# Kernel optimization log

Hardware: AMD Instinct MI355X
Metric: run time of the kernel (lower is better)

The kernel has to match this reference:

```python
import jax, jax.numpy as jnp
import numpy as np

N_VOX = 200_000
C = 64
B, G = 2, 128  # batch size, grid resolution per axis
K = 27         # 3x3x3 kernel volume
EPS = 1e-5


def _build_coords_and_kernel_map(seed=0):
    """Build unique voxel coords on a [B,G,G,G] grid and the 27-offset kernel map.

    nbr[i, k] = row index of the voxel at coord[i] + offset[k], or N_VOX if absent
    (sentinel row that gathers zeros). This mirrors MinkowskiEngine's
    coordinate-hash in/out kernel maps for a stride-1 conv.
    """
    rng = np.random.default_rng(seed)
    total = B * G * G * G
    keys = np.sort(rng.choice(total, size=N_VOX, replace=False).astype(np.int64))
    z = keys % G
    y = (keys // G) % G
    x = (keys // (G * G)) % G
    b = keys // (G * G * G)
    offs = [(dx, dy, dz) for dx in (-1, 0, 1) for dy in (-1, 0, 1) for dz in (-1, 0, 1)]
    nbr = np.full((N_VOX, K), N_VOX, dtype=np.int64)
    for k, (dx, dy, dz) in enumerate(offs):
        nx, ny, nz = x + dx, y + dy, z + dz
        valid = (nx >= 0) & (nx < G) & (ny >= 0) & (ny < G) & (nz >= 0) & (nz < G)
        nkey = ((b * G + nx) * G + ny) * G + nz
        pos = np.clip(np.searchsorted(keys, nkey), 0, N_VOX - 1)
        found = valid & (keys[pos] == nkey)
        nbr[:, k] = np.where(found, pos, N_VOX)
    return jnp.asarray(nbr)


def setup_inputs() -> dict:
    key = jax.random.key(0)
    ks = jax.random.split(key, 12)
    w_scale = 1.0 / np.sqrt(K * C)
    inp = {
        "feats": jax.random.normal(ks[0], (N_VOX, C), jnp.float32),
        "nbr": _build_coords_and_kernel_map(),
        "W1": jax.random.normal(ks[1], (K, C, C), jnp.float32) * w_scale,
        "g1": 1.0 + 0.1 * jax.random.normal(ks[2], (C,), jnp.float32),
        "b1": 0.1 * jax.random.normal(ks[3], (C,), jnp.float32),
        "m1": 0.1 * jax.random.normal(ks[4], (C,), jnp.float32),
        "v1": jax.random.uniform(ks[5], (C,), jnp.float32, 0.5, 1.5),
        "W2": jax.random.normal(ks[6], (K, C, C), jnp.float32) * w_scale,
        "g2": 1.0 + 0.1 * jax.random.normal(ks[7], (C,), jnp.float32),
        "b2": 0.1 * jax.random.normal(ks[8], (C,), jnp.float32),
        "m2": 0.1 * jax.random.normal(ks[9], (C,), jnp.float32),
        "v2": jax.random.uniform(ks[10], (C,), jnp.float32, 0.5, 1.5),
    }
    return inp


def _bn(x, g, b, m, v):
    # MinkowskiBatchNorm, eval mode: per-channel affine with running stats
    return (x - m) * (g * jax.lax.rsqrt(v + EPS)) + b


def _sparse_conv(feats, nbr, W):
    # gather-GEMM-scatter sparse 3D conv over the precomputed kernel map.
    # Sentinel index N_VOX gathers the appended zero row (missing neighbor).
    fpad = jnp.concatenate([feats, jnp.zeros((1, feats.shape[1]), feats.dtype)], axis=0)
    out = jnp.zeros((feats.shape[0], W.shape[2]), feats.dtype)
    for k in range(W.shape[0]):  # fixed 27-tap loop (structural, not data dim)
        out = out + fpad[nbr[:, k]] @ W[k]
    return out


def reference(feats, nbr, W1, g1, b1, m1, v1, W2, g2, b2, m2, v2):
    h = jax.nn.relu(_bn(_sparse_conv(feats, nbr, W1), g1, b1, m1, v1))
    h = _bn(_sparse_conv(h, nbr, W2), g2, b2, m2, v2)
    # in_channels == out_channels and stride == 1 -> identity shortcut
    return jax.nn.relu(h + feats)
```

## Files before the change

kernel.cpp:

```cpp
#include <hip/hip_runtime.h>
#include <hip/hip_bf16.h>

#define NVOX 200000
#define NTAP 27
#define NSTR 68
#define OSTR 68

typedef __bf16          bf16x8 __attribute__((ext_vector_type(8)));
typedef unsigned short  u16x8  __attribute__((ext_vector_type(8)));
typedef float           f32x4  __attribute__((ext_vector_type(4)));

#define ROWB        128
#define FB_BYTES    ((size_t)(NVOX + 1) * ROWB)
#define WSHUF_BYTES (NTAP * 2 * 4 * 64 * 16)
#define FB_OFF      0
#define H_OFF       (FB_BYTES)
#define WS1_OFF     (2 * FB_BYTES)
#define WS2_OFF     (WS1_OFF + WSHUF_BYTES)
#define FLAG_OFF    (WS2_OFF + WSHUF_BYTES)

static __device__ __forceinline__ unsigned short f2bf_bits(float f) {
    __hip_bfloat16 h = __float2bfloat16(f);
    union { __hip_bfloat16 h; unsigned short u; } u; u.h = h; return u.u;
}
static __device__ __forceinline__ float bf2f(unsigned short s) {
    union { float f; unsigned u; } u; u.u = ((unsigned)s) << 16; return u.f;
}
static __device__ __forceinline__ float ld_param(const void* p, int c, int isbf) {
    return isbf ? bf2f(((const unsigned short*)p)[c]) : ((const float*)p)[c];
}
static __device__ __forceinline__ int wave_isbf(const unsigned* v1w) {
    int l = threadIdx.x & 63;
    int ok = 1;
    if (l < 32) {
        unsigned w = v1w[l], lo = w & 0xFFFFu, hi = w >> 16;
        ok = (lo >= 0x3F00u && lo <= 0x3FC0u && hi >= 0x3F00u && hi <= 0x3FC0u);
    }
    return __all(ok);
}

__global__ __launch_bounds__(256)
void prep_kernel(const void* __restrict__ feats,
                 const void* __restrict__ W1, const void* __restrict__ W2,
                 const unsigned* __restrict__ v1w, const unsigned* __restrict__ nbrw,
                 uint4* __restrict__ fbuf, uint4* __restrict__ hbuf,
                 uint4* __restrict__ Ws1, uint4* __restrict__ Ws2,
                 int* __restrict__ flags) {
    const int bx = blockIdx.x;
    if (bx < 6250) {
        const int isbf = wave_isbf(v1w);
        size_t t = (size_t)bx * 256 + threadIdx.x;
        if (isbf) {
            fbuf[t] = ((const uint4*)feats)[t];
        } else {
            float4 a = ((const float4*)feats)[2 * t];
            float4 b = ((const float4*)feats)[2 * t + 1];
            union { uint4 q; unsigned short u[8]; } o;
            o.u[0] = f2bf_bits(a.x); o.u[1] = f2bf_bits(a.y);
            o.u[2] = f2bf_bits(a.z); o.u[3] = f2bf_bits(a.w);
            o.u[4] = f2bf_bits(b.x); o.u[5] = f2bf_bits(b.y);
            o.u[6] = f2bf_bits(b.z); o.u[7] = f2bf_bits(b.w);
            fbuf[t] = o.q;
        }
    } else if (bx < 6358) {
        const int isbf = wave_isbf(v1w);
        int t = (bx - 6250) * 256 + threadIdx.x;
        const void* W = (t < 13824) ? W1 : W2;
        uint4* Ws     = (t < 13824) ? Ws1 : Ws2;
        int f = (t < 13824) ? t : t - 13824;
        int k  = f / 512;
        int r  = f % 512;
        int kc = r / 256;
        int r2 = r % 256;
        int nc = r2 / 64;
        int l  = r2 % 64;
        int quad = l >> 4, li = l & 15;
        unsigned short tmp[8];
#pragma unroll
        for (int j = 0; j < 8; ++j) {
            int off = k * 4096 + (kc * 32 + quad * 8 + j) * 64 + (nc * 16 + li);
            tmp[j] = isbf ? ((const unsigned short*)W)[off]
                          : f2bf_bits(((const float*)W)[off]);
        }
        uint4 v;
        v.x = (unsigned)tmp[0] | ((unsigned)tmp[1] << 16);
        v.y = (unsigned)tmp[2] | ((unsigned)tmp[3] << 16);
        v.z = (unsigned)tmp[4] | ((unsigned)tmp[5] << 16);
        v.w = (unsigned)tmp[6] | ((unsigned)tmp[7] << 16);
        Ws[f] = v;
    } else {
        int t = threadIdx.x;
        if (t < 64) {
            int isbf = wave_isbf(v1w);
            int n64ok = 1;
#pragma unroll
            for (int i = 0; i < 8; ++i)
                if (nbrw[2 * (t * 8 + i) + 1] != 0u) n64ok = 0;
            int n64 = __all(n64ok);
            if (t == 0) { flags[0] = isbf; flags[1] = n64; }
        }
        uint4 z = make_uint4(0u, 0u, 0u, 0u);
        if (t >= 64 && t < 72) fbuf[(size_t)NVOX * 8 + (t - 64)] = z;
        if (t >= 72 && t < 80) hbuf[(size_t)NVOX * 8 + (t - 72)] = z;
    }
}

#define STAGE(kk, bp) do {                                                  \
    int idx_ = nbrLDS[(kk) * NSTR + srow];                                  \
    const uint4* rp_ = srcV + (size_t)idx_ * 8;                             \
    uint4 v0_ = rp_[sf0];                                                   \
    uint4 v1_ = rp_[sf0 + 4];                                               \
    (bp)[ws0] = v0_;                                                        \
    (bp)[ws1] = v1_;                                                        \
} while (0)

#define LOADB(kk, B0, B1) do {                                              \
    B0 = Ws[(kk) * 512 + w * 64 + l];                                       \
    B1 = Ws[(kk) * 512 + 256 + w * 64 + l];                                 \
} while (0)

#define COMPUTE(kk, bp, B0, B1) do {                                        \
    _Pragma("unroll")                                                       \
    for (int g = 0; g < 4; ++g) {                                           \
        if ((mg[g] >> (kk)) & 1) {                                          \
            bf16x8 a0_ = *(const bf16x8*)((bp) + ro0[g]);                   \
            bf16x8 a1_ = *(const bf16x8*)((bp) + ro1[g]);                   \
            acc[g] = __builtin_amdgcn_mfma_f32_16x16x32_bf16(a0_, B0, acc[g], 0, 0, 0); \
            acc[g] = __builtin_amdgcn_mfma_f32_16x16x32_bf16(a1_, B1, acc[g], 0, 0, 0); \
        }                                                                   \
    }                                                                       \
} while (0)

__global__ __launch_bounds__(256, 6)
void conv_bn_kernel(const uint4* __restrict__ srcV,
                    const void* __restrict__ nbr,
                    const bf16x8* __restrict__ Ws,
                    const void* __restrict__ gg, const void* __restrict__ bb,
                    const void* __restrict__ mm, const void* __restrict__ vv,
                    const u16x8* __restrict__ resid,
                    const int* __restrict__ flags,
                    void* __restrict__ dst, int final_out) {
    __shared__ uint4 sm[1484];
    __shared__ int maskLDS[4];
    int*   nbrLDS = (int*)sm;
    uint4* at0    = sm + 459;
    uint4* at1    = at0 + 512;
    float* outLDS = (float*)sm;

    const int tid  = threadIdx.x;
    const int base = blockIdx.x * 64;
    const int isbf = flags[0];
    const int n64  = flags[1];

    if (tid < 4) maskLDS[tid] = 0;
    {
        for (int i = tid; i < NTAP * 64; i += 256) {
            int mvox = i / NTAP;
            int ktap = i - mvox * NTAP;
            long gi = (long)base * NTAP + i;
            int idx = n64 ? (int)((const long long*)nbr)[gi] : ((const int*)nbr)[gi];
            nbrLDS[ktap * NSTR + mvox] = idx;
        }
    }
    __syncthreads();

    if (tid < NTAP * 4) {
        int k = tid >> 2, g = tid & 3;
        const int4* p = (const int4*)&nbrLDS[k * NSTR + g * 16];
        int4 a = p[0], b = p[1], c = p[2], d = p[3];
        int mn = min(min(min(a.x, a.y), min(a.z, a.w)),
                     min(min(min(b.x, b.y), min(b.z, b.w)),
                         min(min(min(c.x, c.y), min(c.z, c.w)),
                             min(min(d.x, d.y), min(d.z, d.w)))));
        if (mn < NVOX) atomicOr(&maskLDS[g], 1 << k);
    }
    __syncthreads();

    const int w = tid >> 6, l = tid & 63;
    const int quad = l >> 4, li = l & 15;

    int mg[4];
#pragma unroll
    for (int g = 0; g < 4; ++g) mg[g] = __builtin_amdgcn_readfirstlane(maskLDS[g]);

    const int srow = tid & 63;
    const int sf0  = tid >> 6;
    const int ws0  = srow * 8 + ((sf0 + srow) & 7);
    const int ws1  = srow * 8 + ((sf0 + 4 + srow) & 7);
    int ro0[4], ro1[4];
#pragma unroll
    for (int g = 0; g < 4; ++g) {
        int row = g * 16 + li;
        ro0[g] = row * 8 + ((quad + row) & 7);
        ro1[g] = row * 8 + ((quad + 4 + row) & 7);
    }

    f32x4 acc[4];
#pragma unroll
    for (int g = 0; g < 4; ++g) acc[g] = (f32x4){0.f, 0.f, 0.f, 0.f};

    bf16x8 xB0, xB1, yB0, yB1;
    STAGE(0, at0);
    LOADB(0, xB0, xB1);
    __syncthreads();

    for (int k = 0; k < 26; k += 2) {
        STAGE(k + 1, at1);
        LOADB(k + 1, yB0, yB1);
        COMPUTE(k, at0, xB0, xB1);
        __syncthreads();
        STAGE(k + 2, at0);
        LOADB(k + 2, xB0, xB1);
        COMPUTE(k + 1, at1, yB0, yB1);
        __syncthreads();
    }
    COMPUTE(26, at0, xB0, xB1);

    const int c = w * 16 + li;
    float scale = ld_param(gg, c, isbf) * rsqrtf(ld_param(vv, c, isbf) + 1e-5f);
    float offs  = ld_param(bb, c, isbf) - ld_param(mm, c, isbf) * scale;

    __syncthreads();
#pragma unroll
    for (int g = 0; g < 4; ++g)
#pragma unroll
        for (int r = 0; r < 4; ++r)
            outLDS[(g * 16 + quad * 4 + r) * OSTR + c] = acc[g][r] * scale + offs;
    __syncthreads();

    {
        int trow = tid >> 2, cc = tid & 3;
        long grow = base + trow;
        const float4* lp = (const float4*)&outLDS[trow * OSTR + cc * 16];
        float4 q0 = lp[0], q1 = lp[1], q2 = lp[2], q3 = lp[3];
        float vals[16] = {q0.x, q0.y, q0.z, q0.w, q1.x, q1.y, q1.z, q1.w,
                          q2.x, q2.y, q2.z, q2.w, q3.x, q3.y, q3.z, q3.w};

        if (resid) {
            const u16x8* rp = resid + grow * 8 + cc * 2;
            u16x8 r0 = rp[0], r1 = rp[1];
#pragma unroll
            for (int j = 0; j < 8; ++j) { vals[j] += bf2f(r0[j]); vals[8 + j] += bf2f(r1[j]); }
        }
#pragma unroll
        for (int j = 0; j < 16; ++j) vals[j] = fmaxf(vals[j], 0.f);

        const int store_bf = (!final_out) || isbf;
        if (store_bf) {
            u16x8 o0, o1;
#pragma unroll
            for (int j = 0; j < 8; ++j) { o0[j] = f2bf_bits(vals[j]); o1[j] = f2bf_bits(vals[8 + j]); }
            u16x8* dp = (u16x8*)dst + grow * 8 + cc * 2;
            dp[0] = o0; dp[1] = o1;
        } else {
            float4* dp = (float4*)dst + grow * 16 + cc * 4;
            dp[0] = (float4){vals[0], vals[1], vals[2], vals[3]};
            dp[1] = (float4){vals[4], vals[5], vals[6], vals[7]};
            dp[2] = (float4){vals[8], vals[9], vals[10], vals[11]};
            dp[3] = (float4){vals[12], vals[13], vals[14], vals[15]};
        }
    }
}

extern "C" void kernel_launch(void* const* d_in, const int* in_sizes, int n_in,
                              void* d_out, int out_size, void* d_ws, size_t ws_size,
                              hipStream_t stream) {
    const void* feats = d_in[0];
    const void* nbr   = d_in[1];
    const void* W1    = d_in[2];
    const void* g1    = d_in[3];
    const void* b1    = d_in[4];
    const void* m1    = d_in[5];
    const void* v1    = d_in[6];
    const void* W2    = d_in[7];
    const void* g2    = d_in[8];
    const void* b2    = d_in[9];
    const void* m2    = d_in[10];
    const void* v2    = d_in[11];

    char* ws = (char*)d_ws;
    uint4* fbuf = (uint4*)(ws + FB_OFF);
    uint4* hbuf = (uint4*)(ws + H_OFF);
    uint4* Ws1  = (uint4*)(ws + WS1_OFF);
    uint4* Ws2  = (uint4*)(ws + WS2_OFF);
    int*   flags = (int*)(ws + FLAG_OFF);

    prep_kernel<<<dim3(6359), dim3(256), 0, stream>>>(
        feats, W1, W2, (const unsigned*)v1, (const unsigned*)nbr,
        fbuf, hbuf, Ws1, Ws2, flags);

    conv_bn_kernel<<<dim3(NVOX / 64), dim3(256), 0, stream>>>(
        fbuf, nbr, (const bf16x8*)Ws1, g1, b1, m1, v1,
        nullptr, flags, hbuf, 0);

    conv_bn_kernel<<<dim3(NVOX / 64), dim3(256), 0, stream>>>(
        hbuf, nbr, (const bf16x8*)Ws2, g2, b2, m2, v2,
        (const u16x8*)fbuf, flags, d_out, 1);
}
```

Baseline: 270.0 us.

## Fuse fp32-to-bf16 feature conversion into conv gather and prefetch neighbor rows into registers

Drops the separate pass that converted the whole fp32 feature tensor to a bf16 buffer. The first conv now gathers fp32 neighbor rows directly and converts them before writing to LDS, and the residual add reads fp32 feats directly. Missing neighbors point at a shared zero row, so the padded buffers are no longer needed. The gather is reorganized into global loads into registers issued one tap ahead, with the LDS write after the MFMA compute, to overlap gather latency with compute. This raises register pressure (launch bounds occupancy hint lowered from 6 to 5), and the first conv now gathers twice as many bytes per neighbor row.

```diff
diff --git a/kernel.cpp b/kernel.cpp
--- a/kernel.cpp
+++ b/kernel.cpp
@@ -11,13 +11,13 @@
 typedef float           f32x4  __attribute__((ext_vector_type(4)));
 
 #define ROWB        128
-#define FB_BYTES    ((size_t)(NVOX + 1) * ROWB)
+#define H_BYTES     ((size_t)NVOX * ROWB)
 #define WSHUF_BYTES (NTAP * 2 * 4 * 64 * 16)
-#define FB_OFF      0
-#define H_OFF       (FB_BYTES)
-#define WS1_OFF     (2 * FB_BYTES)
+#define H_OFF       0
+#define WS1_OFF     (H_BYTES)
 #define WS2_OFF     (WS1_OFF + WSHUF_BYTES)
-#define FLAG_OFF    (WS2_OFF + WSHUF_BYTES)
+#define ZROW_OFF    (WS2_OFF + WSHUF_BYTES)
+#define FLAG_OFF    (ZROW_OFF + 512)
 
 static __device__ __forceinline__ unsigned short f2bf_bits(float f) {
     __hip_bfloat16 h = __float2bfloat16(f);
@@ -40,58 +40,14 @@
 }
 
 __global__ __launch_bounds__(256)
-void prep_kernel(const void* __restrict__ feats,
-                 const void* __restrict__ W1, const void* __restrict__ W2,
+void prep_kernel(const void* __restrict__ W1, const void* __restrict__ W2,
                  const unsigned* __restrict__ v1w, const unsigned* __restrict__ nbrw,
-                 uint4* __restrict__ fbuf, uint4* __restrict__ hbuf,
                  uint4* __restrict__ Ws1, uint4* __restrict__ Ws2,
-                 int* __restrict__ flags) {
-    const int bx = blockIdx.x;
-    if (bx < 6250) {
-        const int isbf = wave_isbf(v1w);
-        size_t t = (size_t)bx * 256 + threadIdx.x;
-        if (isbf) {
-            fbuf[t] = ((const uint4*)feats)[t];
-        } else {
-            float4 a = ((const float4*)feats)[2 * t];
-            float4 b = ((const float4*)feats)[2 * t + 1];
-            union { uint4 q; unsigned short u[8]; } o;
-            o.u[0] = f2bf_bits(a.x); o.u[1] = f2bf_bits(a.y);
-            o.u[2] = f2bf_bits(a.z); o.u[3] = f2bf_bits(a.w);
-            o.u[4] = f2bf_bits(b.x); o.u[5] = f2bf_bits(b.y);
-            o.u[6] = f2bf_bits(b.z); o.u[7] = f2bf_bits(b.w);
-            fbuf[t] = o.q;
-        }
-    } else if (bx < 6358) {
-        const int isbf = wave_isbf(v1w);
-        int t = (bx - 6250) * 256 + threadIdx.x;
-        const void* W = (t < 13824) ? W1 : W2;
-        uint4* Ws     = (t < 13824) ? Ws1 : Ws2;
-        int f = (t < 13824) ? t : t - 13824;
-        int k  = f / 512;
-        int r  = f % 512;
-        int kc = r / 256;
-        int r2 = r % 256;
-        int nc = r2 / 64;
-        int l  = r2 % 64;
-        int quad = l >> 4, li = l & 15;
-        unsigned short tmp[8];
-#pragma unroll
-        for (int j = 0; j < 8; ++j) {
-            int off = k * 4096 + (kc * 32 + quad * 8 + j) * 64 + (nc * 16 + li);
-            tmp[j] = isbf ? ((const unsigned short*)W)[off]
-                          : f2bf_bits(((const float*)W)[off]);
-        }
-        uint4 v;
-        v.x = (unsigned)tmp[0] | ((unsigned)tmp[1] << 16);
-        v.y = (unsigned)tmp[2] | ((unsigned)tmp[3] << 16);
-        v.z = (unsigned)tmp[4] | ((unsigned)tmp[5] << 16);
-        v.w = (unsigned)tmp[6] | ((unsigned)tmp[7] << 16);
-        Ws[f] = v;
-    } else {
+                 int* __restrict__ flags, uint4* __restrict__ zrow) {
+    const int isbf = wave_isbf(v1w);
+    if (blockIdx.x == 108) {
         int t = threadIdx.x;
         if (t < 64) {
-            int isbf = wave_isbf(v1w);
             int n64ok = 1;
 #pragma unroll
             for (int i = 0; i < 8; ++i)
@@ -99,20 +55,62 @@
             int n64 = __all(n64ok);
             if (t == 0) { flags[0] = isbf; flags[1] = n64; }
         }
-        uint4 z = make_uint4(0u, 0u, 0u, 0u);
-        if (t >= 64 && t < 72) fbuf[(size_t)NVOX * 8 + (t - 64)] = z;
-        if (t >= 72 && t < 80) hbuf[(size_t)NVOX * 8 + (t - 72)] = z;
-    }
-}
-
-#define STAGE(kk, bp) do {                                                  \
+        if (t < 32) zrow[t] = make_uint4(0u, 0u, 0u, 0u);
+        return;
+    }
+    int t = blockIdx.x * 256 + threadIdx.x;
+    const void* W = (t < 13824) ? W1 : W2;
+    uint4* Ws     = (t < 13824) ? Ws1 : Ws2;
+    int f = (t < 13824) ? t : t - 13824;
+    int k  = f / 512;
+    int r  = f % 512;
+    int kc = r / 256;
+    int r2 = r % 256;
+    int nc = r2 / 64;
+    int l  = r2 % 64;
+    int quad = l >> 4, li = l & 15;
+    unsigned short tmp[8];
+#pragma unroll
+    for (int j = 0; j < 8; ++j) {
+        int off = k * 4096 + (kc * 32 + quad * 8 + j) * 64 + (nc * 16 + li);
+        tmp[j] = isbf ? ((const unsigned short*)W)[off]
+                      : f2bf_bits(((const float*)W)[off]);
+    }
+    uint4 v;
+    v.x = (unsigned)tmp[0] | ((unsigned)tmp[1] << 16);
+    v.y = (unsigned)tmp[2] | ((unsigned)tmp[3] << 16);
+    v.z = (unsigned)tmp[4] | ((unsigned)tmp[5] << 16);
+    v.w = (unsigned)tmp[6] | ((unsigned)tmp[7] << 16);
+    Ws[f] = v;
+}
+
+#define GLOAD(kk, RB0, RB1, RF0, RF1, RF2, RF3) do {                        \
     int idx_ = nbrLDS[(kk) * NSTR + srow];                                  \
-    const uint4* rp_ = srcV + (size_t)idx_ * 8;                             \
-    uint4 v0_ = rp_[sf0];                                                   \
-    uint4 v1_ = rp_[sf0 + 4];                                               \
-    (bp)[ws0] = v0_;                                                        \
-    (bp)[ws1] = v1_;                                                        \
-} while (0)
+    if (!src_f32) {                                                         \
+        const uint4* rp_ = (idx_ < NVOX) ?                                  \
+            (const uint4*)src + (size_t)idx_ * 8 : (const uint4*)zrow;      \
+        RB0 = rp_[sf0]; RB1 = rp_[sf0 + 4];                                 \
+    } else {                                                                \
+        const float4* rp_ = (idx_ < NVOX) ?                                 \
+            (const float4*)src + (size_t)idx_ * 16 : (const float4*)zrow;   \
+        RF0 = rp_[sf0 * 2]; RF1 = rp_[sf0 * 2 + 1];                         \
+        RF2 = rp_[sf0 * 2 + 8]; RF3 = rp_[sf0 * 2 + 9];                     \
+    } } while (0)
+
+#define LWRITE(bp, RB0, RB1, RF0, RF1, RF2, RF3) do {                       \
+    if (!src_f32) { (bp)[ws0] = RB0; (bp)[ws1] = RB1; }                     \
+    else {                                                                  \
+        union { uint4 q; unsigned short u[8]; } o0_, o1_;                   \
+        o0_.u[0] = f2bf_bits(RF0.x); o0_.u[1] = f2bf_bits(RF0.y);           \
+        o0_.u[2] = f2bf_bits(RF0.z); o0_.u[3] = f2bf_bits(RF0.w);           \
+        o0_.u[4] = f2bf_bits(RF1.x); o0_.u[5] = f2bf_bits(RF1.y);           \
+        o0_.u[6] = f2bf_bits(RF1.z); o0_.u[7] = f2bf_bits(RF1.w);           \
+        o1_.u[0] = f2bf_bits(RF2.x); o1_.u[1] = f2bf_bits(RF2.y);           \
+        o1_.u[2] = f2bf_bits(RF2.z); o1_.u[3] = f2bf_bits(RF2.w);           \
+        o1_.u[4] = f2bf_bits(RF3.x); o1_.u[5] = f2bf_bits(RF3.y);           \
+        o1_.u[6] = f2bf_bits(RF3.z); o1_.u[7] = f2bf_bits(RF3.w);           \
+        (bp)[ws0] = o0_.q; (bp)[ws1] = o1_.q;                               \
+    } } while (0)
 
 #define LOADB(kk, B0, B1) do {                                              \
     B0 = Ws[(kk) * 512 + w * 64 + l];                                       \
@@ -131,13 +129,14 @@
     }                                                                       \
 } while (0)
 
-__global__ __launch_bounds__(256, 6)
-void conv_bn_kernel(const uint4* __restrict__ srcV,
+__global__ __launch_bounds__(256, 5)
+void conv_bn_kernel(const void* __restrict__ src, int src_raw,
                     const void* __restrict__ nbr,
                     const bf16x8* __restrict__ Ws,
                     const void* __restrict__ gg, const void* __restrict__ bb,
                     const void* __restrict__ mm, const void* __restrict__ vv,
-                    const u16x8* __restrict__ resid,
+                    const void* __restrict__ resid,
+                    const void* __restrict__ zrow,
                     const int* __restrict__ flags,
                     void* __restrict__ dst, int final_out) {
     __shared__ uint4 sm[1484];
@@ -151,6 +150,7 @@
     const int base = blockIdx.x * 64;
     const int isbf = flags[0];
     const int n64  = flags[1];
+    const int src_f32 = src_raw && !isbf;
 
     if (tid < 4) maskLDS[tid] = 0;
     {
@@ -200,18 +200,28 @@
     for (int g = 0; g < 4; ++g) acc[g] = (f32x4){0.f, 0.f, 0.f, 0.f};
 
     bf16x8 xB0, xB1, yB0, yB1;
-    STAGE(0, at0);
+    uint4  XB0, XB1, YB0, YB1;
+    float4 XF0, XF1, XF2, XF3, YF0, YF1, YF2, YF3;
+
+    GLOAD(0, XB0, XB1, XF0, XF1, XF2, XF3);
+    GLOAD(1, YB0, YB1, YF0, YF1, YF2, YF3);
+    LWRITE(at0, XB0, XB1, XF0, XF1, XF2, XF3);
     LOADB(0, xB0, xB1);
     __syncthreads();
 
     for (int k = 0; k < 26; k += 2) {
-        STAGE(k + 1, at1);
+        GLOAD(k + 2, XB0, XB1, XF0, XF1, XF2, XF3);
         LOADB(k + 1, yB0, yB1);
         COMPUTE(k, at0, xB0, xB1);
+        LWRITE(at1, YB0, YB1, YF0, YF1, YF2, YF3);
         __syncthreads();
-        STAGE(k + 2, at0);
+        {
+            int kn = (k + 3 <= 26) ? k + 3 : 26;
+            GLOAD(kn, YB0, YB1, YF0, YF1, YF2, YF3);
+        }
         LOADB(k + 2, xB0, xB1);
         COMPUTE(k + 1, at1, yB0, yB1);
+        LWRITE(at0, XB0, XB1, XF0, XF1, XF2, XF3);
         __syncthreads();
     }
     COMPUTE(26, at0, xB0, xB1);
@@ -237,10 +247,19 @@
                           q2.x, q2.y, q2.z, q2.w, q3.x, q3.y, q3.z, q3.w};
 
         if (resid) {
-            const u16x8* rp = resid + grow * 8 + cc * 2;
-            u16x8 r0 = rp[0], r1 = rp[1];
-#pragma unroll
-            for (int j = 0; j < 8; ++j) { vals[j] += bf2f(r0[j]); vals[8 + j] += bf2f(r1[j]); }
+            if (isbf) {
+                const u16x8* rp = (const u16x8*)resid + grow * 8 + cc * 2;
+                u16x8 r0 = rp[0], r1 = rp[1];
+#pragma unroll
+                for (int j = 0; j < 8; ++j) { vals[j] += bf2f(r0[j]); vals[8 + j] += bf2f(r1[j]); }
+            } else {
+                const float4* rp = (const float4*)resid + grow * 16 + cc * 4;
+                float4 p0 = rp[0], p1 = rp[1], p2 = rp[2], p3 = rp[3];
+                vals[0] += p0.x;  vals[1] += p0.y;  vals[2] += p0.z;  vals[3] += p0.w;
+                vals[4] += p1.x;  vals[5] += p1.y;  vals[6] += p1.z;  vals[7] += p1.w;
+                vals[8] += p2.x;  vals[9] += p2.y;  vals[10] += p2.z; vals[11] += p2.w;
+                vals[12] += p3.x; vals[13] += p3.y; vals[14] += p3.z; vals[15] += p3.w;
+            }
         }
 #pragma unroll
         for (int j = 0; j < 16; ++j) vals[j] = fmaxf(vals[j], 0.f);
@@ -279,21 +298,20 @@
     const void* v2    = d_in[11];
 
     char* ws = (char*)d_ws;
-    uint4* fbuf = (uint4*)(ws + FB_OFF);
     uint4* hbuf = (uint4*)(ws + H_OFF);
     uint4* Ws1  = (uint4*)(ws + WS1_OFF);
     uint4* Ws2  = (uint4*)(ws + WS2_OFF);
+    uint4* zrow = (uint4*)(ws + ZROW_OFF);
     int*   flags = (int*)(ws + FLAG_OFF);
 
-    prep_kernel<<<dim3(6359), dim3(256), 0, stream>>>(
-        feats, W1, W2, (const unsigned*)v1, (const unsigned*)nbr,
-        fbuf, hbuf, Ws1, Ws2, flags);
+    prep_kernel<<<dim3(109), dim3(256), 0, stream>>>(
+        W1, W2, (const unsigned*)v1, (const unsigned*)nbr, Ws1, Ws2, flags, zrow);
 
     conv_bn_kernel<<<dim3(NVOX / 64), dim3(256), 0, stream>>>(
-        fbuf, nbr, (const bf16x8*)Ws1, g1, b1, m1, v1,
-        nullptr, flags, hbuf, 0);
+        feats, 1, nbr, (const bf16x8*)Ws1, g1, b1, m1, v1,
+        nullptr, zrow, flags, hbuf, 0);
 
     conv_bn_kernel<<<dim3(NVOX / 64), dim3(256), 0, stream>>>(
-        hbuf, nbr, (const bf16x8*)Ws2, g2, b2, m2, v2,
-        (const u16x8*)fbuf, flags, d_out, 1);
-}
+        hbuf, 0, nbr, (const bf16x8*)Ws2, g2, b2, m2, v2,
+        feats, zrow, flags, d_out, 1);
+}
```

New measurement: 699.3 us. 2.59x slower.

## Make each wave own 16 voxels, gathering A directly to registers without LDS

Applied to the files above, without the earlier changes.

The conv kernel now gives each wave its own 16 output rows across all 64 output channels. Each wave gathers neighbor rows straight from global memory into registers and loads all four weight column groups per tap, so the LDS staging and the block-wide barrier on every tap go away. Each wave skips taps where none of its 16 voxels has a neighbor, which is a finer skip than the old per-16-row-group mask, and it double-buffers in registers. The cost is four times more weight loads per block and higher register pressure: launch bounds occupancy drops from 6 to 4, and gather latency is now hidden only by the register prefetch.

```diff
diff --git a/kernel.cpp b/kernel.cpp
--- a/kernel.cpp
+++ b/kernel.cpp
@@ -3,14 +3,14 @@
 
 #define NVOX 200000
 #define NTAP 27
-#define NSTR 68
 #define OSTR 68
+#define WSTR 1088
+#define ROWB 128
 
 typedef __bf16          bf16x8 __attribute__((ext_vector_type(8)));
 typedef unsigned short  u16x8  __attribute__((ext_vector_type(8)));
 typedef float           f32x4  __attribute__((ext_vector_type(4)));
 
-#define ROWB        128
 #define FB_BYTES    ((size_t)(NVOX + 1) * ROWB)
 #define WSHUF_BYTES (NTAP * 2 * 4 * 64 * 16)
 #define FB_OFF      0
@@ -28,6 +28,9 @@
 }
 static __device__ __forceinline__ float ld_param(const void* p, int c, int isbf) {
     return isbf ? bf2f(((const unsigned short*)p)[c]) : ((const float*)p)[c];
+}
+static __device__ __forceinline__ bf16x8 asbf(uint4 v) {
+    union { uint4 q; bf16x8 b; } u; u.q = v; return u.b;
 }
 static __device__ __forceinline__ int wave_isbf(const unsigned* v1w) {
     int l = threadIdx.x & 63;
@@ -105,142 +108,117 @@
     }
 }
 
-#define STAGE(kk, bp) do {                                                  \
-    int idx_ = nbrLDS[(kk) * NSTR + srow];                                  \
-    const uint4* rp_ = srcV + (size_t)idx_ * 8;                             \
-    uint4 v0_ = rp_[sf0];                                                   \
-    uint4 v1_ = rp_[sf0 + 4];                                               \
-    (bp)[ws0] = v0_;                                                        \
-    (bp)[ws1] = v1_;                                                        \
+#define PF(...) PF_(__VA_ARGS__)
+#define PF_(kk, A0, A1, B0, B1, B2, B3, B4, B5, B6, B7) do {                \
+    int idx_ = nbrW[(l & 15) * NTAP + (kk)];                                \
+    const uint4* rp_ = (const uint4*)(srcB + (size_t)idx_ * ROWB);          \
+    A0 = rp_[quad]; A1 = rp_[quad + 4];                                     \
+    const uint4* wp_ = Ws + (kk) * 512 + l;                                 \
+    B0 = wp_[0];   B1 = wp_[256];                                           \
+    B2 = wp_[64];  B3 = wp_[320];                                           \
+    B4 = wp_[128]; B5 = wp_[384];                                           \
+    B6 = wp_[192]; B7 = wp_[448];                                           \
 } while (0)
 
-#define LOADB(kk, B0, B1) do {                                              \
-    B0 = Ws[(kk) * 512 + w * 64 + l];                                       \
-    B1 = Ws[(kk) * 512 + 256 + w * 64 + l];                                 \
+#define DOMF(...) DOMF_(__VA_ARGS__)
+#define DOMF_(A0, A1, B0, B1, B2, B3, B4, B5, B6, B7) do {                  \
+    acc0 = __builtin_amdgcn_mfma_f32_16x16x32_bf16(asbf(A0), asbf(B0), acc0, 0, 0, 0); \
+    acc1 = __builtin_amdgcn_mfma_f32_16x16x32_bf16(asbf(A0), asbf(B2), acc1, 0, 0, 0); \
+    acc2 = __builtin_amdgcn_mfma_f32_16x16x32_bf16(asbf(A0), asbf(B4), acc2, 0, 0, 0); \
+    acc3 = __builtin_amdgcn_mfma_f32_16x16x32_bf16(asbf(A0), asbf(B6), acc3, 0, 0, 0); \
+    acc0 = __builtin_amdgcn_mfma_f32_16x16x32_bf16(asbf(A1), asbf(B1), acc0, 0, 0, 0); \
+    acc1 = __builtin_amdgcn_mfma_f32_16x16x32_bf16(asbf(A1), asbf(B3), acc1, 0, 0, 0); \
+    acc2 = __builtin_amdgcn_mfma_f32_16x16x32_bf16(asbf(A1), asbf(B5), acc2, 0, 0, 0); \
+    acc3 = __builtin_amdgcn_mfma_f32_16x16x32_bf16(asbf(A1), asbf(B7), acc3, 0, 0, 0); \
 } while (0)
 
-#define COMPUTE(kk, bp, B0, B1) do {                                        \
-    _Pragma("unroll")                                                       \
-    for (int g = 0; g < 4; ++g) {                                           \
-        if ((mg[g] >> (kk)) & 1) {                                          \
-            bf16x8 a0_ = *(const bf16x8*)((bp) + ro0[g]);                   \
-            bf16x8 a1_ = *(const bf16x8*)((bp) + ro1[g]);                   \
-            acc[g] = __builtin_amdgcn_mfma_f32_16x16x32_bf16(a0_, B0, acc[g], 0, 0, 0); \
-            acc[g] = __builtin_amdgcn_mfma_f32_16x16x32_bf16(a1_, B1, acc[g], 0, 0, 0); \
-        }                                                                   \
-    }                                                                       \
-} while (0)
-
-__global__ __launch_bounds__(256, 6)
+#define XSET XA0, XA1, XB0, XB1, XB2, XB3, XB4, XB5, XB6, XB7
+#define YSET YA0, YA1, YB0, YB1, YB2, YB3, YB4, YB5, YB6, YB7
+
+__global__ __launch_bounds__(256, 4)
 void conv_bn_kernel(const uint4* __restrict__ srcV,
                     const void* __restrict__ nbr,
-                    const bf16x8* __restrict__ Ws,
+                    const uint4* __restrict__ Ws,
                     const void* __restrict__ gg, const void* __restrict__ bb,
                     const void* __restrict__ mm, const void* __restrict__ vv,
                     const u16x8* __restrict__ resid,
                     const int* __restrict__ flags,
                     void* __restrict__ dst, int final_out) {
-    __shared__ uint4 sm[1484];
-    __shared__ int maskLDS[4];
-    int*   nbrLDS = (int*)sm;
-    uint4* at0    = sm + 459;
-    uint4* at1    = at0 + 512;
-    float* outLDS = (float*)sm;
-
+    __shared__ int smi[4 * WSTR];
     const int tid  = threadIdx.x;
+    const int w    = tid >> 6, l = tid & 63;
+    const int quad = l >> 4, li = l & 15;
     const int base = blockIdx.x * 64;
+    const int wrow = base + w * 16;
     const int isbf = flags[0];
     const int n64  = flags[1];
-
-    if (tid < 4) maskLDS[tid] = 0;
+    int* nbrW = smi + w * WSTR;
+    const char* srcB = (const char*)srcV;
+
+    if (!n64) {
+        const int* np = (const int*)nbr + (long)wrow * NTAP;
+        for (int i = l; i < 16 * NTAP; i += 64) nbrW[i] = np[i];
+    } else {
+        const long long* np = (const long long*)nbr + (long)wrow * NTAP;
+        for (int i = l; i < 16 * NTAP; i += 64) nbrW[i] = (int)np[i];
+    }
+
+    unsigned msk = 0;
+    for (int t = 0; t < NTAP; ++t) {
+        int idx = nbrW[(l & 15) * NTAP + t];
+        if (__any(idx < NVOX)) msk |= 1u << t;
+    }
+
+    f32x4 acc0 = {0.f, 0.f, 0.f, 0.f}, acc1 = {0.f, 0.f, 0.f, 0.f};
+    f32x4 acc2 = {0.f, 0.f, 0.f, 0.f}, acc3 = {0.f, 0.f, 0.f, 0.f};
+    uint4 XA0, XA1, XB0, XB1, XB2, XB3, XB4, XB5, XB6, XB7;
+    uint4 YA0, YA1, YB0, YB1, YB2, YB3, YB4, YB5, YB6, YB7;
+
+    unsigned mrem = msk;
+    int ka = __ffs(mrem) - 1; mrem &= mrem - 1;
+    PF(ka, XSET);
+    for (;;) {
+        int kb = -1;
+        if (mrem) { kb = __ffs(mrem) - 1; mrem &= mrem - 1; }
+        if (kb < 0) { DOMF(XSET); break; }
+        PF(kb, YSET);
+        DOMF(XSET);
+        int kc = -1;
+        if (mrem) { kc = __ffs(mrem) - 1; mrem &= mrem - 1; }
+        if (kc < 0) { DOMF(YSET); break; }
+        PF(kc, XSET);
+        DOMF(YSET);
+    }
+
+    float scl[4], ofs[4];
+#pragma unroll
+    for (int s = 0; s < 4; ++s) {
+        int c = s * 16 + li;
+        scl[s] = ld_param(gg, c, isbf) * rsqrtf(ld_param(vv, c, isbf) + 1e-5f);
+        ofs[s] = ld_param(bb, c, isbf) - ld_param(mm, c, isbf) * scl[s];
+    }
+
+    float* outW = (float*)nbrW;
+#define EPI(s, accv) do { _Pragma("unroll")                                 \
+    for (int r = 0; r < 4; ++r)                                             \
+        outW[(quad * 4 + r) * OSTR + (s) * 16 + li] = accv[r] * scl[s] + ofs[s]; \
+    } while (0)
+    EPI(0, acc0); EPI(1, acc1); EPI(2, acc2); EPI(3, acc3);
+#undef EPI
+
     {
-        for (int i = tid; i < NTAP * 64; i += 256) {
-            int mvox = i / NTAP;
-            int ktap = i - mvox * NTAP;
-            long gi = (long)base * NTAP + i;
-            int idx = n64 ? (int)((const long long*)nbr)[gi] : ((const int*)nbr)[gi];
-            nbrLDS[ktap * NSTR + mvox] = idx;
-        }
-    }
-    __syncthreads();
-
-    if (tid < NTAP * 4) {
-        int k = tid >> 2, g = tid & 3;
-        const int4* p = (const int4*)&nbrLDS[k * NSTR + g * 16];
-        int4 a = p[0], b = p[1], c = p[2], d = p[3];
-        int mn = min(min(min(a.x, a.y), min(a.z, a.w)),
-                     min(min(min(b.x, b.y), min(b.z, b.w)),
-                         min(min(min(c.x, c.y), min(c.z, c.w)),
-                             min(min(d.x, d.y), min(d.z, d.w)))));
-        if (mn < NVOX) atomicOr(&maskLDS[g], 1 << k);
-    }
-    __syncthreads();
-
-    const int w = tid >> 6, l = tid & 63;
-    const int quad = l >> 4, li = l & 15;
-
-    int mg[4];
-#pragma unroll
-    for (int g = 0; g < 4; ++g) mg[g] = __builtin_amdgcn_readfirstlane(maskLDS[g]);
-
-    const int srow = tid & 63;
-    const int sf0  = tid >> 6;
-    const int ws0  = srow * 8 + ((sf0 + srow) & 7);
-    const int ws1  = srow * 8 + ((sf0 + 4 + srow) & 7);
-    int ro0[4], ro1[4];
-#pragma unroll
-    for (int g = 0; g < 4; ++g) {
-        int row = g * 16 + li;
-        ro0[g] = row * 8 + ((quad + row) & 7);
-        ro1[g] = row * 8 + ((quad + 4 + row) & 7);
-    }
-
-    f32x4 acc[4];
-#pragma unroll
-    for (int g = 0; g < 4; ++g) acc[g] = (f32x4){0.f, 0.f, 0.f, 0.f};
-
-    bf16x8 xB0, xB1, yB0, yB1;
-    STAGE(0, at0);
-    LOADB(0, xB0, xB1);
-    __syncthreads();
-
-    for (int k = 0; k < 26; k += 2) {
-        STAGE(k + 1, at1);
-        LOADB(k + 1, yB0, yB1);
-        COMPUTE(k, at0, xB0, xB1);
-        __syncthreads();
-        STAGE(k + 2, at0);
-        LOADB(k + 2, xB0, xB1);
-        COMPUTE(k + 1, at1, yB0, yB1);
-        __syncthreads();
-    }
-    COMPUTE(26, at0, xB0, xB1);
-
-    const int c = w * 16 + li;
-    float scale = ld_param(gg, c, isbf) * rsqrtf(ld_param(vv, c, isbf) + 1e-5f);
-    float offs  = ld_param(bb, c, isbf) - ld_param(mm, c, isbf) * scale;
-
-    __syncthreads();
-#pragma unroll
-    for (int g = 0; g < 4; ++g)
-#pragma unroll
-        for (int r = 0; r < 4; ++r)
-            outLDS[(g * 16 + quad * 4 + r) * OSTR + c] = acc[g][r] * scale + offs;
-    __syncthreads();
-
-    {
-        int trow = tid >> 2, cc = tid & 3;
-        long grow = base + trow;
-        const float4* lp = (const float4*)&outLDS[trow * OSTR + cc * 16];
+        int trow = l >> 2, cc = l & 3;
+        long grow = wrow + trow;
+        const float4* lp = (const float4*)&outW[trow * OSTR + cc * 16];
         float4 q0 = lp[0], q1 = lp[1], q2 = lp[2], q3 = lp[3];
         float vals[16] = {q0.x, q0.y, q0.z, q0.w, q1.x, q1.y, q1.z, q1.w,
                           q2.x, q2.y, q2.z, q2.w, q3.x, q3.y, q3.z, q3.w};
 
         if (resid) {
             const u16x8* rp = resid + grow * 8 + cc * 2;
-            u16x8 r0 = rp[0], r1 = rp[1];
-#pragma unroll
-            for (int j = 0; j < 8; ++j) { vals[j] += bf2f(r0[j]); vals[8 + j] += bf2f(r1[j]); }
+            u16x8 r0v = rp[0], r1v = rp[1];
+#pragma unroll
+            for (int j = 0; j < 8; ++j) { vals[j] += bf2f(r0v[j]); vals[8 + j] += bf2f(r1v[j]); }
         }
 #pragma unroll
         for (int j = 0; j < 16; ++j) vals[j] = fmaxf(vals[j], 0.f);
@@ -290,10 +268,10 @@
         fbuf, hbuf, Ws1, Ws2, flags);
 
     conv_bn_kernel<<<dim3(NVOX / 64), dim3(256), 0, stream>>>(
-        fbuf, nbr, (const bf16x8*)Ws1, g1, b1, m1, v1,
+        fbuf, nbr, Ws1, g1, b1, m1, v1,
         nullptr, flags, hbuf, 0);
 
     conv_bn_kernel<<<dim3(NVOX / 64), dim3(256), 0, stream>>>(
-        hbuf, nbr, (const bf16x8*)Ws2, g2, b2, m2, v2,
+        hbuf, nbr, Ws2, g2, b2, m2, v2,
         (const u16x8*)fbuf, flags, d_out, 1);
 }
```

After: 925.5 us. 243% more time.
